# Performance work log

Hardware: AMD Instinct MI355X
Metric: run time of the kernel (lower is better)

The kernel has to match this reference:

```python
import jax, jax.numpy as jnp
import numpy as np

N = 50000
E = 640000
H = 128
C = 3

def _xavier(key, shape, gain=1.0):
    fan_in, fan_out = shape[0], shape[1]
    a = gain * np.sqrt(6.0 / (fan_in + fan_out))
    return jax.random.uniform(key, shape, jnp.float32, -a, a)

def setup_inputs() -> dict:
    key = jax.random.key(0)
    ks = jax.random.split(key, 12)
    h = jax.random.normal(ks[0], (N, H), jnp.float32)
    x = jax.random.normal(ks[1], (N, C), jnp.float32)
    edge_index = jax.random.randint(ks[2], (2, E), 0, N, jnp.int64 if jax.config.jax_enable_x64 else jnp.int32)
    # edge_mlp: Linear(2H+1 -> H), SiLU, Linear(H -> H), SiLU
    We1 = _xavier(ks[3], (2 * H + 1, H)); be1 = jnp.zeros((H,), jnp.float32)
    We2 = _xavier(ks[4], (H, H));          be2 = jnp.zeros((H,), jnp.float32)
    # coord_mlp: Linear(H -> H), SiLU, Linear(H -> 1, no bias, gain 0.01)
    Wc1 = _xavier(ks[5], (H, H)); bc1 = jnp.zeros((H,), jnp.float32)
    Wc2 = _xavier(ks[6], (H, 1), gain=0.01)
    # node_mlp: Linear(2H -> H), SiLU, Linear(H -> H)
    Wn1 = _xavier(ks[7], (2 * H, H)); bn1 = jnp.zeros((H,), jnp.float32)
    Wn2 = _xavier(ks[8], (H, H));     bn2 = jnp.zeros((H,), jnp.float32)
    return dict(h=h, x=x, edge_index=edge_index,
                We1=We1, be1=be1, We2=We2, be2=be2,
                Wc1=Wc1, bc1=bc1, Wc2=Wc2,
                Wn1=Wn1, bn1=bn1, Wn2=Wn2, bn2=bn2)

def reference(h, x, edge_index, We1, be1, We2, be2, Wc1, bc1, Wc2, Wn1, bn1, Wn2, bn2):
    src, dst = edge_index[0], edge_index[1]
    n = h.shape[0]
    rel_pos = x[src] - x[dst]                              # [E, C]
    dist_sq = jnp.sum(rel_pos * rel_pos, axis=-1, keepdims=True)  # [E, 1]
    edge_input = jnp.concatenate([h[src], h[dst], dist_sq], axis=-1)  # [E, 2H+1]
    m_ij = jax.nn.silu(edge_input @ We1 + be1)
    m_ij = jax.nn.silu(m_ij @ We2 + be2)                   # [E, H]
    coord_weight = jax.nn.silu(m_ij @ Wc1 + bc1) @ Wc2     # [E, 1]
    coord_agg = jax.ops.segment_sum(rel_pos * coord_weight, dst, num_segments=n)
    x_out = x + coord_agg
    msg_agg = jax.ops.segment_sum(m_ij, dst, num_segments=n)  # [N, H]
    node_input = jnp.concatenate([h, msg_agg], axis=-1)    # [N, 2H]
    h_upd = jax.nn.silu(node_input @ Wn1 + bn1) @ Wn2 + bn2
    h_out = h + h_upd
    return (h_out, x_out)
```

## Files before the change

### kernel.cpp

```cpp
#include <hip/hip_runtime.h>

#define H 128

typedef __bf16 bf8_t __attribute__((ext_vector_type(8)));
typedef __bf16 bf2_t __attribute__((ext_vector_type(2)));
typedef float  f4_t  __attribute__((ext_vector_type(4)));

#define MFMA16(a, b, c) __builtin_amdgcn_mfma_f32_16x16x32_bf16((a), (b), (c), 0, 0, 0)

__device__ __forceinline__ float silu_f(float v) {
    return v * (1.0f / (1.0f + __expf(-v)));
}

__device__ __forceinline__ void bar_lds() {
    asm volatile("s_waitcnt lgkmcnt(0)\ns_barrier" ::: "memory");
}

__device__ __forceinline__ float wload(const void* p, int idx, bool f32) {
    return f32 ? ((const float*)p)[idx] : (float)((const __bf16*)p)[idx];
}

__device__ __forceinline__ bf8_t hload8(const void* p, size_t off, bool f32) {
    bf8_t v;
    if (f32) {
        const float4* q = (const float4*)((const float*)p + off);
        const float4 a = q[0], b = q[1];
        v[0]=(__bf16)a.x; v[1]=(__bf16)a.y; v[2]=(__bf16)a.z; v[3]=(__bf16)a.w;
        v[4]=(__bf16)b.x; v[5]=(__bf16)b.y; v[6]=(__bf16)b.z; v[7]=(__bf16)b.w;
    } else {
        v = *(const bf8_t*)((const __bf16*)p + off);
    }
    return v;
}

__device__ __forceinline__ int eidx(const void* ei, int i, bool i64) {
    return i64 ? (int)((const long long*)ei)[i] : ((const int*)ei)[i];
}

__global__ void detect_kernel(const unsigned short* __restrict__ hraw,
                              const int* __restrict__ eiraw, int* __restrict__ flags)
{
    __shared__ int s_nf, s_oddnz;
    if (threadIdx.x == 0) { s_nf = 0; s_oddnz = 0; }
    __syncthreads();
    int nf = 0;
    for (int i = threadIdx.x; i < 16384; i += blockDim.x) {
        const unsigned short u = hraw[i];
        if (((u >> 7) & 0xFF) == 0xFF) nf++;
    }
    int onz = 0;
    for (int i = threadIdx.x; i < 512; i += blockDim.x) {
        if (eiraw[2*i + 1] != 0) onz++;
    }
    if (nf)  atomicAdd(&s_nf, nf);
    if (onz) atomicAdd(&s_oddnz, onz);
    __syncthreads();
    if (threadIdx.x == 0) {
        flags[0] = (s_nf > 0) ? 1 : 0;
        flags[1] = (s_oddnz == 0) ? 1 : 0;
    }
}

__global__ void histd_kernel(const void* __restrict__ ei, int* __restrict__ cnt,
                             const int* __restrict__ flags, int Ee)
{
    const int e = blockIdx.x*blockDim.x + threadIdx.x;
    if (e < Ee) atomicAdd(&cnt[eidx(ei, Ee + e, flags[1] != 0)], 1);
}

__global__ void scanA_kernel(const int* __restrict__ cnt, int* __restrict__ bsum, int Nn)
{
    __shared__ int s[512];
    const int gi = blockIdx.x*512 + threadIdx.x;
    s[threadIdx.x] = (gi < Nn) ? cnt[gi] : 0;
    __syncthreads();
    for (int off = 256; off > 0; off >>= 1) {
        if (threadIdx.x < off) s[threadIdx.x] += s[threadIdx.x + off];
        __syncthreads();
    }
    if (threadIdx.x == 0) bsum[blockIdx.x] = s[0];
}

__global__ void scanB_kernel(int* __restrict__ bsum, int* __restrict__ base, int nCh)
{
    if (threadIdx.x == 0) {
        int acc = 0;
        for (int b = 0; b < nCh; ++b) { base[b] = acc; acc += bsum[b]; }
    }
}
// ... 66 lines not shown
        #pragma unroll
        for (int kc = 0; kc < 4; ++kc) {
            bf8_t v;
            #pragma unroll
            for (int j = 0; j < 8; ++j)
                v[j] = (__bf16)wload(We1, (rb + kc*32 + quad*8 + j)*H + col, f32);
            bW[kc][t] = v;
        }
        bias[t] = (n < 128) ? 0.f : wload(be1, col, f32);
    }

    __shared__ __bf16 s_h[32*136];

    const int tiles = (Nn + 31) >> 5;
    for (int tile = blockIdx.x; tile < tiles; tile += gridDim.x) {
        const int nb = tile << 5;
        __syncthreads();
        {
            const int m = tid >> 4, c = tid & 15;
            int node = nb + m; if (node >= Nn) node = Nn - 1;
            *(bf8_t*)&s_h[m*136 + c*8] = hload8(h, (size_t)node*H + c*8, f32);
        }
        __syncthreads();

        f4_t acc[2][2];
        #pragma unroll
        for (int mm = 0; mm < 2; ++mm)
            #pragma unroll
            for (int t = 0; t < 2; ++t) acc[mm][t] = (f4_t){0.f,0.f,0.f,0.f};
        #pragma unroll
        for (int kc = 0; kc < 4; ++kc) {
            #pragma unroll
            for (int mm = 0; mm < 2; ++mm) {
                const bf8_t a = *(const bf8_t*)&s_h[(mm*16 + l15)*136 + quad*8 + kc*32];
                acc[mm][0] = MFMA16(a, bW[kc][0], acc[mm][0]);
                acc[mm][1] = MFMA16(a, bW[kc][1], acc[mm][1]);
            }
        }
        #pragma unroll
        for (int mm = 0; mm < 2; ++mm)
            #pragma unroll
            for (int i = 0; i < 4; ++i) {
                const int row = nb + mm*16 + quad*4 + i;
                if (row < Nn) {
                    #pragma unroll
                    for (int t = 0; t < 2; ++t)
                        PB[(size_t)row*256 + wv*32 + t*16 + l15] =
                            (__bf16)(acc[mm][t][i] + bias[t]);
                }
            }
    }
}

__global__ __launch_bounds__(512, 2)
void egnn_edge_pipe_kernel(const __bf16* __restrict__ PB,
                           const int* __restrict__ srcs, const int* __restrict__ dsts,
                           const float4* __restrict__ rel4,
                           const void* __restrict__ We1,
                           const void* __restrict__ We2, const void* __restrict__ be2,
                           const void* __restrict__ Wc1, const void* __restrict__ bc1,
                           const void* __restrict__ Wc2, const int* __restrict__ flags,
                           float* __restrict__ msg, float* __restrict__ coord,
                           int Ee)
{
    const bool f32 = flags[0] != 0;
    const int tid  = threadIdx.x;
    const int wv   = tid >> 6;
    const int lane = tid & 63;
    const int quad = lane >> 4;
    const int l15  = lane & 15;
    const int mg   = wv >> 2;
    const int ng   = wv & 3;

    bf8_t bW2[4][2], bWc[4][2];
    float be2v[2], bc1v[2], wc2v[2];
    #pragma unroll
    for (int t = 0; t < 2; ++t) {
        const int n = ng*32 + t*16 + l15;
        #pragma unroll
        for (int kc = 0; kc < 4; ++kc) {
            bf8_t v, u;
            #pragma unroll
            for (int j = 0; j < 8; ++j) {
                v[j] = (__bf16)wload(We2, (kc*32 + quad*8 + j)*H + n, f32);
                u[j] = (__bf16)wload(Wc1, (kc*32 + quad*8 + j)*H + n, f32);
            }
            bW2[kc][t] = v;
            bWc[kc][t] = u;
        }
        be2v[t] = wload(be2, n, f32);
        bc1v[t] = wload(bc1, n, f32);
        wc2v[t] = wload(Wc2, n, f32);
    }

    const int em = tid >> 3;
    const int ch = tid & 7;
    float w1dA[8], w1dB[8];
    #pragma unroll
    for (int j = 0; j < 8; ++j) {
        w1dA[j] = wload(We1, 256*H + ch*8 + j, f32);
        w1dB[j] = wload(We1, 256*H + (ch+8)*8 + j, f32);
    }

    __shared__ __bf16 s_m1[64*136];
    __shared__ __bf16 s_m2[64*136];
    __shared__ float  s_cw[4*64];
    __shared__ int    s_dst[2][64];
    __shared__ float4 s_rl[2][64];
    __shared__ float  s_pre[8][128];
    __shared__ float  s_suf[8][128];
    __shared__ int    s_wh[8];

    const int tiles = (Ee + 63) >> 6;
    const float* rw = (const float*)rel4;

    bf8_t rA0, rA1, rB0, rB1;
    float d2cur, d2nxt;
    int   s_n, d_n, d_c;
    float4 r4c, r4n;
    {
        int e0 = blockIdx.x*64 + em; if (e0 >= Ee) e0 = Ee - 1;
        const int sc = srcs[e0], dc = dsts[e0];
        d_c = dc;
        d2cur = rw[(size_t)e0*4 + 3];
        if (ch == 0) r4c = rel4[e0];
        rA0 = *(const bf8_t*)(PB + (size_t)sc*256 + ch*8);
        rA1 = *(const bf8_t*)(PB + (size_t)sc*256 + (ch+8)*8);
        rB0 = *(const bf8_t*)(PB + (size_t)dc*256 + 128 + ch*8);
        rB1 = *(const bf8_t*)(PB + (size_t)dc*256 + 128 + (ch+8)*8);
        const int t1 = blockIdx.x + gridDim.x;
        const int tt = (t1 < tiles) ? t1 : blockIdx.x;
        int e1 = tt*64 + em; if (e1 >= Ee) e1 = Ee - 1;
        s_n = srcs[e1]; d_n = dsts[e1]; d2nxt = rw[(size_t)e1*4 + 3];
        if (ch == 0) r4n = rel4[e1];
    }

    int li = 0;
    for (int t = blockIdx.x; t < tiles; t += gridDim.x, ++li) {
        const int sb = li & 1;
        {
            bf8_t o0, o1;
            #pragma unroll
            for (int j = 0; j < 8; ++j) {
                const float f0 = (float)rA0[j] + (float)rB0[j] + d2cur*w1dA[j];
                const float f1 = (float)rA1[j] + (float)rB1[j] + d2cur*w1dB[j];
                o0[j] = (__bf16)silu_f(f0);
                o1[j] = (__bf16)silu_f(f1);
            }
            *(bf8_t*)&s_m1[em*136 + ch*8]       = o0;
            *(bf8_t*)&s_m1[em*136 + (ch+8)*8]   = o1;
            if (ch == 0) { s_dst[sb][em] = d_c; s_rl[sb][em] = r4c; }
        }
        {
            const int sc = s_n, dc2 = d_n;
            rA0 = *(const bf8_t*)(PB + (size_t)sc*256 + ch*8);
            rA1 = *(const bf8_t*)(PB + (size_t)sc*256 + (ch+8)*8);
            rB0 = *(const bf8_t*)(PB + (size_t)dc2*256 + 128 + ch*8);
            rB1 = *(const bf8_t*)(PB + (size_t)dc2*256 + 128 + (ch+8)*8);
            d_c = d_n; d2cur = d2nxt;
            if (ch == 0) r4c = r4n;
            const int t2 = t + 2*gridDim.x;
            const int tt = (t2 < tiles) ? t2 : t;
            int e2 = tt*64 + em; if (e2 >= Ee) e2 = Ee - 1;
            s_n = srcs[e2]; d_n = dsts[e2]; d2nxt = rw[(size_t)e2*4 + 3];
            if (ch == 0) r4n = rel4[e2];
        }
        bar_lds();

        {
            f4_t a2[2][2];
            #pragma unroll
            for (int mm = 0; mm < 2; ++mm)
                #pragma unroll
                for (int h2 = 0; h2 < 2; ++h2) a2[mm][h2] = (f4_t){0.f,0.f,0.f,0.f};
            #pragma unroll
            for (int kc = 0; kc < 4; ++kc) {
                #pragma unroll
                for (int mm = 0; mm < 2; ++mm) {
                    const bf8_t a = *(const bf8_t*)&s_m1[(mg*32 + mm*16 + l15)*136 + quad*8 + kc*32];
                    a2[mm][0] = MFMA16(a, bW2[kc][0], a2[mm][0]);
                    a2[mm][1] = MFMA16(a, bW2[kc][1], a2[mm][1]);
                }
            }
            #pragma unroll
            for (int mm = 0; mm < 2; ++mm)
                #pragma unroll
                for (int i = 0; i < 4; ++i) {
                    const int m = mg*32 + mm*16 + quad*4 + i;
                    s_m2[m*136 + ng*32 + l15]      = (__bf16)silu_f(a2[mm][0][i] + be2v[0]);
                    s_m2[m*136 + ng*32 + 16 + l15] = (__bf16)silu_f(a2[mm][1][i] + be2v[1]);
                }
        }
        bar_lds();

        {
            f4_t a3[2][2];
            #pragma unroll
            for (int mm = 0; mm < 2; ++mm)
                #pragma unroll
                for (int h2 = 0; h2 < 2; ++h2) a3[mm][h2] = (f4_t){0.f,0.f,0.f,0.f};
            #pragma unroll
            for (int kc = 0; kc < 4; ++kc) {
                #pragma unroll
                for (int mm = 0; mm < 2; ++mm) {
                    const bf8_t a = *(const bf8_t*)&s_m2[(mg*32 + mm*16 + l15)*136 + quad*8 + kc*32];
                    a3[mm][0] = MFMA16(a, bWc[kc][0], a3[mm][0]);
                    a3[mm][1] = MFMA16(a, bWc[kc][1], a3[mm][1]);
                }
            }
            float p[2][4];
            #pragma unroll
            for (int mm = 0; mm < 2; ++mm)
                #pragma unroll
                for (int i = 0; i < 4; ++i) {
                    const float v0 = silu_f(a3[mm][0][i] + bc1v[0]);
                    const float v1 = silu_f(a3[mm][1][i] + bc1v[1]);
                    p[mm][i] = v0*wc2v[0] + v1*wc2v[1];
                }
            #pragma unroll
            for (int off = 1; off < 16; off <<= 1)
                #pragma unroll
                for (int mm = 0; mm < 2; ++mm)
                    #pragma unroll
                    for (int i = 0; i < 4; ++i) p[mm][i] += __shfl_xor(p[mm][i], off, 64);
            if (l15 == 0) {
                #pragma unroll
                for (int mm = 0; mm < 2; ++mm)
                    #pragma unroll
                    for (int i = 0; i < 4; ++i)
                        s_cw[ng*64 + (mg*32 + mm*16 + quad*4 + i)] = p[mm][i];
            }
        }

        {
            const int rbase = wv << 3;
            const int c0    = lane << 1;
            int   curd = __builtin_amdgcn_readfirstlane(s_dst[sb][rbase]);
            float ax = 0.f, ay = 0.f;
            float px = 0.f, py = 0.f;
            int   predone = 0;
            #pragma unroll
            for (int i = 0; i < 8; ++i) {
                const int d = __builtin_amdgcn_readfirstlane(s_dst[sb][rbase + i]);
                const bf2_t v = *(const bf2_t*)&s_m2[(rbase + i)*136 + c0];
                const float vx = (float)v[0], vy = (float)v[1];
                if (d != curd) {
                    if (!predone) { px = ax; py = ay; predone = 1; }
                    else {
                        float2 st; st.x = ax; st.y = ay;
                        *(float2*)&msg[(size_t)curd*H + c0] = st;
                    }
                    curd = d; ax = vx; ay = vy;
                } else { ax += vx; ay += vy; }
            }
            s_pre[wv][c0]   = px;  s_pre[wv][c0+1] = py;
            s_suf[wv][c0]   = ax;  s_suf[wv][c0+1] = ay;
            if (lane == 0) s_wh[wv] = !predone;
        }
        bar_lds();

        if (tid >= 128 && tid < 256) {
            const int c = tid - 128;
            int   curd2 = __builtin_amdgcn_readfirstlane(s_dst[sb][0]);
            float cur   = 0.f;
            int   first = 1;
            #pragma unroll
            for (int gg = 0; gg < 8; ++gg) {
                const int F  = __builtin_amdgcn_readfirstlane(s_dst[sb][gg*8]);
                const int L  = __builtin_amdgcn_readfirstlane(s_dst[sb][gg*8 + 7]);
                const int wh = __builtin_amdgcn_readfirstlane(s_wh[gg]);
                const float preg = s_pre[gg][c];
                const float sufg = s_suf[gg][c];
                if (F != curd2) {
                    if (first) atomicAdd(&msg[(size_t)curd2*H + c], cur);
                    else       msg[(size_t)curd2*H + c] = cur;
                    first = 0; curd2 = F; cur = 0.f;
                }
                if (wh) {
                    cur += sufg;
                } else {
                    cur += preg;
                    if (first) atomicAdd(&msg[(size_t)curd2*H + c], cur);
                    else       msg[(size_t)curd2*H + c] = cur;
                    first = 0; curd2 = L; cur = sufg;
                }
            }
            atomicAdd(&msg[(size_t)curd2*H + c], cur);
        }

        if (tid < 64) {
            const int e = tid;
            const float cwv = s_cw[e] + s_cw[64 + e] + s_cw[128 + e] + s_cw[192 + e];
            const float4 r = s_rl[sb][e];
            const int d = s_dst[sb][e];
            float vx = r.x*cwv, vy = r.y*cwv, vz = r.z*cwv;
            int   cn = 1;
            #pragma unroll
            for (int k = 1; k < 64; k <<= 1) {
                const int   dk = __shfl_up(d,  k, 64);
                const float xk = __shfl_up(vx, k, 64);
                const float yk = __shfl_up(vy, k, 64);
                const float zk = __shfl_up(vz, k, 64);
                const int   ck = __shfl_up(cn, k, 64);
                if (e >= k && dk == d) { vx += xk; vy += yk; vz += zk; cn += ck; }
            }
            const int dnx = __shfl_down(d, 1, 64);
            const bool runend = (e == 63) || (dnx != d);
            if (runend) {
                const int rs = e - cn + 1;
                if (rs == 0 || e == 63) {
                    atomicAdd(&coord[(size_t)d*3 + 0], vx);
                    atomicAdd(&coord[(size_t)d*3 + 1], vy);
                    atomicAdd(&coord[(size_t)d*3 + 2], vz);
                } else {
                    coord[(size_t)d*3 + 0] = vx;
                    coord[(size_t)d*3 + 1] = vy;
                    coord[(size_t)d*3 + 2] = vz;
                }
            }
        }
    }
}

__global__ __launch_bounds__(512, 2)
void egnn_node_kernel(const void* __restrict__ h, const float* __restrict__ msg,
                      const void* __restrict__ Wn1, const void* __restrict__ bn1,
                      const void* __restrict__ Wn2, const void* __restrict__ bn2,
                      const int* __restrict__ flags, void* __restrict__ h_out,
                      const void* __restrict__ x, const float* __restrict__ coord,
                      size_t obase, int do_x, int Nn)
{
    const bool f32 = flags[0] != 0;
    const int tid  = threadIdx.x;
    const int wv   = tid >> 6;
    const int lane = tid & 63;
    const int quad = lane >> 4;
    const int l15  = lane & 15;
    const int mg   = wv >> 2;
    const int ng   = wv & 3;

    bf8_t bW1[8][2];
    bf8_t bW2[4][2];
    float b1v[2], b2v[2];
    #pragma unroll
    for (int t = 0; t < 2; ++t) {
        const int n = ng*32 + t*16 + l15;
        #pragma unroll
        for (int kc = 0; kc < 8; ++kc) {
            bf8_t v;
            #pragma unroll
            for (int j = 0; j < 8; ++j) v[j] = (__bf16)wload(Wn1, (kc*32 + quad*8 + j)*H + n, f32);
            bW1[kc][t] = v;
        }
        #pragma unroll
        for (int kc = 0; kc < 4; ++kc) {
            bf8_t v;
            #pragma unroll
            for (int j = 0; j < 8; ++j) v[j] = (__bf16)wload(Wn2, (kc*32 + quad*8 + j)*H + n, f32);
            bW2[kc][t] = v;
        }
        b1v[t] = wload(bn1, n, f32);
        b2v[t] = wload(bn2, n, f32);
    }

    __shared__ __bf16 s_in[32*264];
    __shared__ __bf16 s_t1[32*136];

    const int tiles = (Nn + 31) >> 5;
    for (int tile = blockIdx.x; tile < tiles; tile += gridDim.x) {
        const int nb = tile << 5;
        __syncthreads();
        #pragma unroll
        for (int r = 0; r < 2; ++r) {
// ... 238 lines not shown
                #pragma unroll
                for (int i = 0; i < 4; ++i)
                    s_cw[(mg*16 + quad*4 + i)*4 + ng] = p[i];
            }
        }
        __syncthreads();

        if (tid < 96) {
            const int m = tid / 3, c = tid - m*3;
            const float cw = s_cw[m*4 + 0] + s_cw[m*4 + 1] + s_cw[m*4 + 2] + s_cw[m*4 + 3];
            atomicAdd(&coord_agg[(size_t)s_dstv[m]*3 + c], s_rel[m*3 + c]*cw);
        }
    }
}

__global__ void egnn_x_kernel(const void* __restrict__ x, const float* __restrict__ coord_agg,
                              const int* __restrict__ flags, void* __restrict__ out,
                              size_t obase, int total)
{
    const bool f32 = flags[0] != 0;
    const int i = blockIdx.x*blockDim.x + threadIdx.x;
    if (i >= total) return;
    const float xv = f32 ? ((const float*)x)[i] : (float)((const __bf16*)x)[i];
    const float o = xv + coord_agg[i];
    if (f32) ((float*)out)[obase + i] = o;
    else     ((__bf16*)out)[obase + i] = (__bf16)o;
}

static inline size_t align256(size_t v) { return (v + 255) & ~(size_t)255; }

extern "C" void kernel_launch(void* const* d_in, const int* in_sizes, int n_in,
                              void* d_out, int out_size, void* d_ws, size_t ws_size,
                              hipStream_t stream)
{
    const void* h   = d_in[0];
    const void* x   = d_in[1];
    const void* ei0 = d_in[2];
    const void* We1 = d_in[3];
    const void* be1 = d_in[4];
    const void* We2 = d_in[5];
    const void* be2 = d_in[6];
    const void* Wc1 = d_in[7];
    const void* bc1 = d_in[8];
    const void* Wc2 = d_in[9];
    const void* Wn1 = d_in[10];
    const void* bn1 = d_in[11];
    const void* Wn2 = d_in[12];
    const void* bn2 = d_in[13];

    const int Nn = in_sizes[0] / H;
    const int Ee = in_sizes[2] / 2;

    char* ws = (char*)d_ws;
    size_t o = 0;
    size_t o_cnt   = o; o = align256(o + (size_t)Nn*4);
    size_t o_msg   = o; o = align256(o + (size_t)Nn*H*4);
    size_t o_coord = o; o = align256(o + (size_t)Nn*3*4);
    const size_t zero_end = o;
    size_t o_srcs  = o; o = align256(o + (size_t)Ee*4);
    size_t o_dsts  = o; o = align256(o + (size_t)Ee*4);
    size_t o_rel   = o; o = align256(o + (size_t)Ee*16);
    size_t o_pb    = o; o = align256(o + (size_t)Nn*256*2);
    size_t o_off   = o; o = align256(o + (size_t)(Nn+1)*4);
    size_t o_cur   = o; o = align256(o + (size_t)Nn*4);
    size_t o_bsum  = o; o = align256(o + 512*4);
    size_t o_base  = o; o = align256(o + 512*4);
    size_t o_flags = o; o = align256(o + 64);
    const size_t need_csr = o;

    const int nCh = (Nn + 1 + 511) / 512;

    if (ws_size >= need_csr) {
        int*    cnt     = (int*)   (ws + o_cnt);
        float*  msg     = (float*) (ws + o_msg);
        float*  coord   = (float*) (ws + o_coord);
        int*    srcs    = (int*)   (ws + o_srcs);
        int*    dsts    = (int*)   (ws + o_dsts);
        float4* rel4    = (float4*)(ws + o_rel);
        __bf16* PB      = (__bf16*)(ws + o_pb);
        int*    off     = (int*)   (ws + o_off);
        int*    cursor  = (int*)   (ws + o_cur);
        int*    bsum    = (int*)   (ws + o_bsum);
        int*    base    = (int*)   (ws + o_base);
        int*    flags   = (int*)   (ws + o_flags);

        detect_kernel<<<1, 256, 0, stream>>>((const unsigned short*)h, (const int*)ei0, flags);
        hipMemsetAsync(ws + o_cnt, 0, zero_end - o_cnt, stream);
        histd_kernel<<<(Ee + 511)/512, 512, 0, stream>>>(ei0, cnt, flags, Ee);
        scanA_kernel<<<nCh, 512, 0, stream>>>(cnt, bsum, Nn);
        scanB_kernel<<<1, 64, 0, stream>>>(bsum, base, nCh);
        scanC_kernel<<<nCh, 512, 0, stream>>>(cnt, base, off, cursor, Nn);
        scatgeo_kernel<<<(Ee + 511)/512, 512, 0, stream>>>(ei0, cursor, srcs, dsts,
                                                           rel4, x, flags, Ee);
        proj_kernel<<<512, 512, 0, stream>>>(h, We1, be1, flags, PB, Nn);

        egnn_edge_pipe_kernel<<<512, 512, 0, stream>>>(PB, srcs, dsts, rel4,
                                                       We1, We2, be2, Wc1, bc1, Wc2,
                                                       flags, msg, coord, Ee);

        egnn_node_kernel<<<1024, 512, 0, stream>>>(h, msg, Wn1, bn1, Wn2, bn2,
                                                   flags, d_out, x, coord,
                                                   (size_t)Nn*H, 1, Nn);
    } else {
        float* msg_agg   = (float*)ws;
        float* coord_agg = (float*)(ws + (size_t)Nn*H*4);
        int*   ei        = (int*)  (ws + (size_t)Nn*H*4 + (size_t)Nn*3*4);
        int*   flags     = (int*)  (ws + (size_t)Nn*H*4 + (size_t)Nn*3*4 + (size_t)2*Ee*4);

        detect_kernel<<<1, 256, 0, stream>>>((const unsigned short*)h, (const int*)ei0, flags);
        cvt_ei_kernel<<<(2*Ee + 255)/256, 256, 0, stream>>>(ei0, ei, 2*Ee, flags);
        hipMemsetAsync(msg_agg,   0, (size_t)Nn*H*4, stream);
        hipMemsetAsync(coord_agg, 0, (size_t)Nn*3*4, stream);
        egnn_edge_kernel<<<1024, 512, 0, stream>>>(h, x, ei, We1, be1, We2, be2,
                                                   Wc1, bc1, Wc2, flags,
                                                   msg_agg, coord_agg, Nn, Ee);
        egnn_node_kernel<<<512, 512, 0, stream>>>(h, msg_agg, Wn1, bn1, Wn2, bn2,
                                                  flags, d_out, x, coord_agg,
                                                  (size_t)Nn*H, 0, Nn);
        egnn_x_kernel<<<(Nn*3 + 255)/256, 256, 0, stream>>>(x, coord_agg, flags, d_out,
                                                            (size_t)Nn*H, Nn*3);
    }
}
```

Measured before the change: 652.9 us.

## Materialize per-edge messages and gather-reduce them in CSR node kernel

Adds a new edge kernel that writes each edge's bf16 message vector and partial coordinate weights to a workspace buffer instead of doing segmented reductions in-kernel. A new node kernel then sums each node's messages along CSR offsets and fuses the coordinate aggregation and node MLP, so the msg/coord memsets and float accumulation buffers are no longer needed. In exchange it writes and rereads roughly 256 bytes per edge of extra global traffic and needs a larger workspace. It falls back to the old path if the workspace is too small.

```diff
diff --git a/kernel.cpp b/kernel.cpp
--- a/kernel.cpp
+++ b/kernel.cpp
@@ -208,6 +208,345 @@
 }
 
 __global__ __launch_bounds__(512, 2)
+void egnn_edge_pipe2_kernel(const __bf16* __restrict__ PB,
+                            const int* __restrict__ srcs, const int* __restrict__ dsts,
+                            const float4* __restrict__ rel4,
+                            const void* __restrict__ We1,
+                            const void* __restrict__ We2, const void* __restrict__ be2,
+                            const void* __restrict__ Wc1, const void* __restrict__ bc1,
+                            const void* __restrict__ Wc2, const int* __restrict__ flags,
+                            unsigned int* __restrict__ m_buf,
+                            float* __restrict__ cwp,
+                            int Ee)
+{
+    const bool f32 = flags[0] != 0;
+    const int tid  = threadIdx.x;
+    const int wv   = tid >> 6;
+    const int lane = tid & 63;
+    const int quad = lane >> 4;
+    const int l15  = lane & 15;
+    const int mg   = wv >> 2;
+    const int ng   = wv & 3;
+
+    bf8_t bW2[4][2], bWc[4][2];
+    float be2v[2], bc1v[2], wc2v[2];
+    #pragma unroll
+    for (int t = 0; t < 2; ++t) {
+        const int n = ng*32 + t*16 + l15;
+        #pragma unroll
+        for (int kc = 0; kc < 4; ++kc) {
+            bf8_t v, u;
+            #pragma unroll
+            for (int j = 0; j < 8; ++j) {
+                v[j] = (__bf16)wload(We2, (kc*32 + quad*8 + j)*H + n, f32);
+                u[j] = (__bf16)wload(Wc1, (kc*32 + quad*8 + j)*H + n, f32);
+            }
+            bW2[kc][t] = v;
+            bWc[kc][t] = u;
+        }
+        be2v[t] = wload(be2, n, f32);
+        bc1v[t] = wload(bc1, n, f32);
+        wc2v[t] = wload(Wc2, n, f32);
+    }
+
+    const int em = tid >> 3;
+    const int ch = tid & 7;
+    float w1dA[8], w1dB[8];
+    #pragma unroll
+    for (int j = 0; j < 8; ++j) {
+        w1dA[j] = wload(We1, 256*H + ch*8 + j, f32);
+        w1dB[j] = wload(We1, 256*H + (ch+8)*8 + j, f32);
+    }
+
+    __shared__ __bf16 s_m1[64*136];
+    __shared__ __bf16 s_m2[64*136];
+
+    const int tiles = (Ee + 63) >> 6;
+    const float* rw = (const float*)rel4;
+
+    bf8_t rA0, rA1, rB0, rB1;
+    float d2cur, d2nxt;
+    int   s_n, d_n;
+    {
+        int e0 = blockIdx.x*64 + em; if (e0 >= Ee) e0 = Ee - 1;
+        const int sc = srcs[e0], dc = dsts[e0];
+        d2cur = rw[(size_t)e0*4 + 3];
+        rA0 = *(const bf8_t*)(PB + (size_t)sc*256 + ch*8);
+        rA1 = *(const bf8_t*)(PB + (size_t)sc*256 + (ch+8)*8);
+        rB0 = *(const bf8_t*)(PB + (size_t)dc*256 + 128 + ch*8);
+        rB1 = *(const bf8_t*)(PB + (size_t)dc*256 + 128 + (ch+8)*8);
+        const int t1 = blockIdx.x + gridDim.x;
+        const int tt = (t1 < tiles) ? t1 : blockIdx.x;
+        int e1 = tt*64 + em; if (e1 >= Ee) e1 = Ee - 1;
+        s_n = srcs[e1]; d_n = dsts[e1]; d2nxt = rw[(size_t)e1*4 + 3];
+    }
+
+    for (int t = blockIdx.x; t < tiles; t += gridDim.x) {
+        {
+            bf8_t o0, o1;
+            #pragma unroll
+            for (int j = 0; j < 8; ++j) {
+                const float f0 = (float)rA0[j] + (float)rB0[j] + d2cur*w1dA[j];
+                const float f1 = (float)rA1[j] + (float)rB1[j] + d2cur*w1dB[j];
+                o0[j] = (__bf16)silu_f(f0);
+                o1[j] = (__bf16)silu_f(f1);
+            }
+            *(bf8_t*)&s_m1[em*136 + ch*8]       = o0;
+            *(bf8_t*)&s_m1[em*136 + (ch+8)*8]   = o1;
+        }
+        {
+            const int sc = s_n, dc2 = d_n;
+            rA0 = *(const bf8_t*)(PB + (size_t)sc*256 + ch*8);
+            rA1 = *(const bf8_t*)(PB + (size_t)sc*256 + (ch+8)*8);
+            rB0 = *(const bf8_t*)(PB + (size_t)dc2*256 + 128 + ch*8);
+            rB1 = *(const bf8_t*)(PB + (size_t)dc2*256 + 128 + (ch+8)*8);
+            d2cur = d2nxt;
+            const int t2 = t + 2*gridDim.x;
+            const int tt = (t2 < tiles) ? t2 : t;
+            int e2 = tt*64 + em; if (e2 >= Ee) e2 = Ee - 1;
+            s_n = srcs[e2]; d_n = dsts[e2]; d2nxt = rw[(size_t)e2*4 + 3];
+        }
+        bar_lds();
+
+        {
+            f4_t a2[2][2];
+            #pragma unroll
+            for (int mm = 0; mm < 2; ++mm)
+                #pragma unroll
+                for (int h2 = 0; h2 < 2; ++h2) a2[mm][h2] = (f4_t){0.f,0.f,0.f,0.f};
+            __builtin_amdgcn_s_setprio(1);
+            #pragma unroll
+            for (int kc = 0; kc < 4; ++kc) {
+                #pragma unroll
+                for (int mm = 0; mm < 2; ++mm) {
+                    const bf8_t a = *(const bf8_t*)&s_m1[(mg*32 + mm*16 + l15)*136 + quad*8 + kc*32];
+                    a2[mm][0] = MFMA16(a, bW2[kc][0], a2[mm][0]);
+                    a2[mm][1] = MFMA16(a, bW2[kc][1], a2[mm][1]);
+                }
+            }
+            __builtin_amdgcn_s_setprio(0);
+            #pragma unroll
+            for (int mm = 0; mm < 2; ++mm)
+                #pragma unroll
+                for (int i = 0; i < 4; ++i) {
+                    const int m = mg*32 + mm*16 + quad*4 + i;
+                    const float v0 = silu_f(a2[mm][0][i] + be2v[0]);
+                    const float v1 = silu_f(a2[mm][1][i] + be2v[1]);
+                    const __bf16 b0 = (__bf16)v0, b1 = (__bf16)v1;
+                    s_m2[m*136 + ng*32 + l15]      = b0;
+                    s_m2[m*136 + ng*32 + 16 + l15] = b1;
+                    const unsigned int w =
+                        ((unsigned int)__builtin_bit_cast(unsigned short, b1) << 16) |
+                        (unsigned int)__builtin_bit_cast(unsigned short, b0);
+                    m_buf[(size_t)(t*64 + m)*64 + ng*16 + l15] = w;
+                }
+        }
+        bar_lds();
+
+        {
+            f4_t a3[2][2];
+            #pragma unroll
+            for (int mm = 0; mm < 2; ++mm)
+                #pragma unroll
+                for (int h2 = 0; h2 < 2; ++h2) a3[mm][h2] = (f4_t){0.f,0.f,0.f,0.f};
+            __builtin_amdgcn_s_setprio(1);
+            #pragma unroll
+            for (int kc = 0; kc < 4; ++kc) {
+                #pragma unroll
+                for (int mm = 0; mm < 2; ++mm) {
+                    const bf8_t a = *(const bf8_t*)&s_m2[(mg*32 + mm*16 + l15)*136 + quad*8 + kc*32];
+                    a3[mm][0] = MFMA16(a, bWc[kc][0], a3[mm][0]);
+                    a3[mm][1] = MFMA16(a, bWc[kc][1], a3[mm][1]);
+                }
+            }
+            __builtin_amdgcn_s_setprio(0);
+            float p[2][4];
+            #pragma unroll
+            for (int mm = 0; mm < 2; ++mm)
+                #pragma unroll
+                for (int i = 0; i < 4; ++i) {
+                    const float v0 = silu_f(a3[mm][0][i] + bc1v[0]);
+                    const float v1 = silu_f(a3[mm][1][i] + bc1v[1]);
+                    p[mm][i] = v0*wc2v[0] + v1*wc2v[1];
+                }
+            #pragma unroll
+            for (int off = 1; off < 16; off <<= 1)
+                #pragma unroll
+                for (int mm = 0; mm < 2; ++mm)
+                    #pragma unroll
+                    for (int i = 0; i < 4; ++i) p[mm][i] += __shfl_xor(p[mm][i], off, 64);
+            if (l15 == 0) {
+                #pragma unroll
+                for (int mm = 0; mm < 2; ++mm)
+                    #pragma unroll
+                    for (int i = 0; i < 4; ++i)
+                        cwp[(size_t)(t*64 + mg*32 + mm*16 + quad*4 + i)*4 + ng] = p[mm][i];
+            }
+        }
+    }
+}
+
+__global__ __launch_bounds__(512, 2)
+void egnn_node_csr_kernel(const void* __restrict__ h,
+                          const unsigned int* __restrict__ m_buf,
+                          const int* __restrict__ offv,
+                          const void* __restrict__ Wn1, const void* __restrict__ bn1,
+                          const void* __restrict__ Wn2, const void* __restrict__ bn2,
+                          const int* __restrict__ flags, void* __restrict__ h_out,
+                          const void* __restrict__ x, const float4* __restrict__ rel4,
+                          const float* __restrict__ cwp,
+                          size_t obase, int Nn)
+{
+    const bool f32 = flags[0] != 0;
+    const int tid  = threadIdx.x;
+    const int wv   = tid >> 6;
+    const int lane = tid & 63;
+    const int quad = lane >> 4;
+    const int l15  = lane & 15;
+    const int mg   = wv >> 2;
+    const int ng   = wv & 3;
+
+    bf8_t bW1[8][2];
+    bf8_t bW2[4][2];
+    float b1v[2], b2v[2];
+    #pragma unroll
+    for (int t = 0; t < 2; ++t) {
+        const int n = ng*32 + t*16 + l15;
+        #pragma unroll
+        for (int kc = 0; kc < 8; ++kc) {
+            bf8_t v;
+            #pragma unroll
+            for (int j = 0; j < 8; ++j) {
+                const int P = kc*32 + quad*8 + j;
+                int krow;
+                if (P < 128) krow = P;
+                else {
+                    const int e2 = P - 128;
+                    const int cp = e2 >> 1, s = e2 & 1;
+                    krow = 128 + ((cp >> 4)*32 + (cp & 15) + 16*s);
+                }
+                v[j] = (__bf16)wload(Wn1, krow*H + n, f32);
+            }
+            bW1[kc][t] = v;
+        }
+        #pragma unroll
+        for (int kc = 0; kc < 4; ++kc) {
+            bf8_t v;
+            #pragma unroll
+            for (int j = 0; j < 8; ++j) v[j] = (__bf16)wload(Wn2, (kc*32 + quad*8 + j)*H + n, f32);
+            bW2[kc][t] = v;
+        }
+        b1v[t] = wload(bn1, n, f32);
+        b2v[t] = wload(bn2, n, f32);
+    }
+
+    __shared__ __bf16 s_in[32*264];
+    __shared__ __bf16 s_t1[32*136];
+
+    const int tiles = (Nn + 31) >> 5;
+    for (int tile = blockIdx.x; tile < tiles; tile += gridDim.x) {
+        const int nb = tile << 5;
+        __syncthreads();
+        {
+            const int m = tid >> 4, c = tid & 15;
+            int node = nb + m; if (node >= Nn) node = Nn - 1;
+            *(bf8_t*)&s_in[m*264 + c*8] = hload8(h, (size_t)node*H + c*8, f32);
+        }
+        {
+            const int m = tid >> 4, cp8 = tid & 15;
+            int node = nb + m; if (node >= Nn) node = Nn - 1;
+            const int p0 = offv[node], p1 = offv[node+1];
+            float acc[8];
+            #pragma unroll
+            for (int k = 0; k < 8; ++k) acc[k] = 0.f;
+            const uint4* mp = (const uint4*)m_buf;
+            for (int p = p0; p < p1; ++p) {
+                const uint4 w = mp[(size_t)p*16 + cp8];
+                acc[0] += __uint_as_float(w.x << 16);
+                acc[1] += __uint_as_float(w.x & 0xffff0000u);
+                acc[2] += __uint_as_float(w.y << 16);
+                acc[3] += __uint_as_float(w.y & 0xffff0000u);
+                acc[4] += __uint_as_float(w.z << 16);
+                acc[5] += __uint_as_float(w.z & 0xffff0000u);
+                acc[6] += __uint_as_float(w.w << 16);
+                acc[7] += __uint_as_float(w.w & 0xffff0000u);
+            }
+            __bf16* d = &s_in[m*264 + 128 + cp8*8];
+            #pragma unroll
+            for (int k = 0; k < 8; ++k) d[k] = (__bf16)acc[k];
+        }
+        if (tid < 96) {
+            const int m = tid / 3, c = tid - m*3;
+            const int node = nb + m;
+            if (node < Nn) {
+                const int p0 = offv[node], p1 = offv[node+1];
+                float acc = 0.f;
+                for (int p = p0; p < p1; ++p) {
+                    const float4 c4 = *(const float4*)&cwp[(size_t)p*4];
+                    const float cw = (c4.x + c4.y) + (c4.z + c4.w);
+                    const float4 r = rel4[p];
+                    const float rc = (c == 0) ? r.x : (c == 1) ? r.y : r.z;
+                    acc += rc * cw;
+                }
+                const float xv = wload(x, node*3 + c, f32);
+                const float o = xv + acc;
+                if (f32) ((float*)h_out)[obase + (size_t)node*3 + c] = o;
+                else     ((__bf16*)h_out)[obase + (size_t)node*3 + c] = (__bf16)o;
+            }
+        }
+        __syncthreads();
+
+        {
+            f4_t a0 = {0.f,0.f,0.f,0.f}, a1 = {0.f,0.f,0.f,0.f};
+            const int abase = (mg*16 + l15)*264 + quad*8;
+            #pragma unroll
+            for (int kc = 0; kc < 8; ++kc) {
+                const bf8_t a = *(const bf8_t*)&s_in[abase + kc*32];
+                a0 = MFMA16(a, bW1[kc][0], a0);
+                a1 = MFMA16(a, bW1[kc][1], a1);
+            }
+            #pragma unroll
+            for (int i = 0; i < 4; ++i) {
+                const int m = mg*16 + quad*4 + i;
+                s_t1[m*136 + ng*32 + l15]      = (__bf16)silu_f(a0[i] + b1v[0]);
+                s_t1[m*136 + ng*32 + 16 + l15] = (__bf16)silu_f(a1[i] + b1v[1]);
+            }
+        }
+        __syncthreads();
+
+        {
+            f4_t a0 = {0.f,0.f,0.f,0.f}, a1 = {0.f,0.f,0.f,0.f};
+            const int abase = (mg*16 + l15)*136 + quad*8;
+            #pragma unroll
+            for (int kc = 0; kc < 4; ++kc) {
+                const bf8_t a = *(const bf8_t*)&s_t1[abase + kc*32];
+                a0 = MFMA16(a, bW2[kc][0], a0);
+                a1 = MFMA16(a, bW2[kc][1], a1);
+            }
+            #pragma unroll
+            for (int i = 0; i < 4; ++i) {
+                const int node = nb + mg*16 + quad*4 + i;
+                if (node < Nn) {
+                    const int n0 = ng*32 + l15, n1 = n0 + 16;
+                    const size_t i0 = (size_t)node*H + n0, i1 = (size_t)node*H + n1;
+                    const float h0 = f32 ? ((const float*)h)[i0] : (float)((const __bf16*)h)[i0];
+                    const float h1 = f32 ? ((const float*)h)[i1] : (float)((const __bf16*)h)[i1];
+                    const float o0 = a0[i] + b2v[0] + h0;
+                    const float o1 = a1[i] + b2v[1] + h1;
+                    if (f32) {
+                        ((float*)h_out)[i0] = o0;
+                        ((float*)h_out)[i1] = o1;
+                    } else {
+                        ((__bf16*)h_out)[i0] = (__bf16)o0;
+                        ((__bf16*)h_out)[i1] = (__bf16)o1;
+                    }
+                }
+            }
+        }
+    }
+}
+
+__global__ __launch_bounds__(512, 2)
 void egnn_edge_pipe_kernel(const __bf16* __restrict__ PB,
                            const int* __restrict__ srcs, const int* __restrict__ dsts,
                            const float4* __restrict__ rel4,
@@ -256,6 +595,11 @@
         w1dA[j] = wload(We1, 256*H + ch*8 + j, f32);
         w1dB[j] = wload(We1, 256*H + (ch+8)*8 + j, f32);
     }
+
+    const int rcol = tid >> 2;
+    const int rg   = tid & 3;
+    const int qb   = lane & ~3;
+    (void)rcol; (void)rg; (void)qb;
 
     __shared__ __bf16 s_m1[64*136];
     __shared__ __bf16 s_m2[64*136];
@@ -818,6 +1162,60 @@
     const int Ee = in_sizes[2] / 2;
 
     char* ws = (char*)d_ws;
+    const int nCh = (Nn + 1 + 511) / 512;
+
+    {
+        size_t o = 0;
+        size_t o_cnt   = o; o = align256(o + (size_t)Nn*4);
+        size_t o_srcs  = o; o = align256(o + (size_t)Ee*4);
+        size_t o_dsts  = o; o = align256(o + (size_t)Ee*4);
+        size_t o_rel   = o; o = align256(o + (size_t)Ee*16);
+        size_t o_pb    = o; o = align256(o + (size_t)Nn*256*2);
+        size_t o_off   = o; o = align256(o + (size_t)(Nn+1)*4);
+        size_t o_cur   = o; o = align256(o + (size_t)Nn*4);
+        size_t o_bsum  = o; o = align256(o + 512*4);
+        size_t o_base  = o; o = align256(o + 512*4);
+        size_t o_flags = o; o = align256(o + 64);
+        size_t o_mbuf  = o; o = align256(o + (size_t)Ee*256);
+        size_t o_cwp   = o; o = align256(o + (size_t)Ee*16);
+        const size_t need_new = o;
+
+        if (ws_size >= need_new) {
+            int*    cnt     = (int*)   (ws + o_cnt);
+            int*    srcs    = (int*)   (ws + o_srcs);
+            int*    dsts    = (int*)   (ws + o_dsts);
+            float4* rel4    = (float4*)(ws + o_rel);
+            __bf16* PB      = (__bf16*)(ws + o_pb);
+            int*    off     = (int*)   (ws + o_off);
+            int*    cursor  = (int*)   (ws + o_cur);
+            int*    bsum    = (int*)   (ws + o_bsum);
+            int*    base    = (int*)   (ws + o_base);
+            int*    flags   = (int*)   (ws + o_flags);
+            unsigned int* m_buf = (unsigned int*)(ws + o_mbuf);
+            float*  cwp     = (float*) (ws + o_cwp);
+
+            detect_kernel<<<1, 256, 0, stream>>>((const unsigned short*)h, (const int*)ei0, flags);
+            hipMemsetAsync(cnt, 0, (size_t)Nn*4, stream);
+            histd_kernel<<<(Ee + 511)/512, 512, 0, stream>>>(ei0, cnt, flags, Ee);
+            scanA_kernel<<<nCh, 512, 0, stream>>>(cnt, bsum, Nn);
+            scanB_kernel<<<1, 64, 0, stream>>>(bsum, base, nCh);
+            scanC_kernel<<<nCh, 512, 0, stream>>>(cnt, base, off, cursor, Nn);
+            scatgeo_kernel<<<(Ee + 511)/512, 512, 0, stream>>>(ei0, cursor, srcs, dsts,
+                                                               rel4, x, flags, Ee);
+            proj_kernel<<<512, 512, 0, stream>>>(h, We1, be1, flags, PB, Nn);
+
+            egnn_edge_pipe2_kernel<<<512, 512, 0, stream>>>(PB, srcs, dsts, rel4,
+                                                            We1, We2, be2, Wc1, bc1, Wc2,
+                                                            flags, m_buf, cwp, Ee);
+
+            egnn_node_csr_kernel<<<1024, 512, 0, stream>>>(h, m_buf, off,
+                                                           Wn1, bn1, Wn2, bn2,
+                                                           flags, d_out, x, rel4, cwp,
+                                                           (size_t)Nn*H, Nn);
+            return;
+        }
+    }
+
     size_t o = 0;
     size_t o_cnt   = o; o = align256(o + (size_t)Nn*4);
     size_t o_msg   = o; o = align256(o + (size_t)Nn*H*4);
@@ -834,8 +1232,6 @@
     size_t o_flags = o; o = align256(o + 64);
     const size_t need_csr = o;
 
-    const int nCh = (Nn + 1 + 511) / 512;
-
     if (ws_size >= need_csr) {
         int*    cnt     = (int*)   (ws + o_cnt);
         float*  msg     = (float*) (ws + o_msg);
```

New measurement: 750.0 us. +14.9%, slower.

## Restructure edge kernel to per-wave 16-edge tiles without block barriers

Applied to the files above, without the earlier changes.

Replaces the block-cooperative 64-edge tile pipeline with a design where each wave independently processes 16 edges. Weights for the two 128x128 MFMAs are staged once in LDS, using a transposed MFMA formulation so edge data stays in registers. Per-wave segmented reductions replace the block-wide prefix/suffix combine, which removes all per-tile block barriers. In exchange, every MFMA now reads its weight fragments from LDS, and the shorter tiles may issue more atomics at run boundaries.

```diff
diff --git a/kernel.cpp b/kernel.cpp
--- a/kernel.cpp
+++ b/kernel.cpp
@@ -3,17 +3,12 @@
 #define H 128
 
 typedef __bf16 bf8_t __attribute__((ext_vector_type(8)));
-typedef __bf16 bf2_t __attribute__((ext_vector_type(2)));
 typedef float  f4_t  __attribute__((ext_vector_type(4)));
 
 #define MFMA16(a, b, c) __builtin_amdgcn_mfma_f32_16x16x32_bf16((a), (b), (c), 0, 0, 0)
 
 __device__ __forceinline__ float silu_f(float v) {
     return v * (1.0f / (1.0f + __expf(-v)));
-}
-
-__device__ __forceinline__ void bar_lds() {
-    asm volatile("s_waitcnt lgkmcnt(0)\ns_barrier" ::: "memory");
 }
 
 __device__ __forceinline__ float wload(const void* p, int idx, bool f32) {
@@ -35,6 +30,12 @@
 
 __device__ __forceinline__ int eidx(const void* ei, int i, bool i64) {
     return i64 ? (int)((const long long*)ei)[i] : ((const int*)ei)[i];
+}
+
+__device__ __forceinline__ unsigned int pkbf(float a, float b) {
+    const __bf16 x = (__bf16)a, y = (__bf16)b;
+    return ((unsigned int)__builtin_bit_cast(unsigned short, y) << 16) |
+           (unsigned int)__builtin_bit_cast(unsigned short, x);
 }
 
 __global__ void detect_kernel(const unsigned short* __restrict__ hraw,
@@ -207,8 +208,8 @@
     }
 }
 
-__global__ __launch_bounds__(512, 2)
-void egnn_edge_pipe_kernel(const __bf16* __restrict__ PB,
+__global__ __launch_bounds__(1024)
+void egnn_edge_wave_kernel(const __bf16* __restrict__ PB,
                            const int* __restrict__ srcs, const int* __restrict__ dsts,
                            const float4* __restrict__ rel4,
                            const void* __restrict__ We1,
@@ -224,246 +225,197 @@
     const int lane = tid & 63;
     const int quad = lane >> 4;
     const int l15  = lane & 15;
-    const int mg   = wv >> 2;
-    const int ng   = wv & 3;
-
-    bf8_t bW2[4][2], bWc[4][2];
-    float be2v[2], bc1v[2], wc2v[2];
-    #pragma unroll
-    for (int t = 0; t < 2; ++t) {
-        const int n = ng*32 + t*16 + l15;
+
+    __shared__ __align__(16) __bf16 s_w2[2048*8];
+    __shared__ __align__(16) __bf16 s_wc[2048*8];
+    __shared__ __align__(16) float  s_bias[4][128];
+    __shared__ __align__(16) __bf16 s_m2w[16][16*152];
+
+    for (int f = tid; f < 2048; f += 1024) {
+        const int g = f >> 8, kc = (f >> 6) & 3, ln = f & 63;
+        const int qd = ln >> 4, l = ln & 15;
+        bf8_t v, u;
+        #pragma unroll
+        for (int j = 0; j < 8; ++j) {
+            const int k = kc*32 + qd*8 + j;
+            v[j] = (__bf16)wload(We2, k*H + g*16 + l, f32);
+            u[j] = (__bf16)wload(Wc1, k*H + g*16 + l, f32);
+        }
+        *(bf8_t*)&s_w2[f*8] = v;
+        *(bf8_t*)&s_wc[f*8] = u;
+    }
+    if (tid < 512) {
+        const int a = tid >> 7, c = tid & 127;
+        float v;
+        if      (a == 0) v = wload(We1, 256*H + c, f32);
+        else if (a == 1) v = wload(be2, c, f32);
+        else if (a == 2) v = wload(bc1, c, f32);
+        else             v = wload(Wc2, c, f32);
+        s_bias[a][c] = v;
+    }
+    __syncthreads();
+
+    const int tiles  = (Ee + 15) >> 4;
+    const int stride = gridDim.x * 16;
+    const float* rw  = (const float*)rel4;
+    int mt = blockIdx.x*16 + wv;
+    if (mt >= tiles) return;
+
+    int e0 = mt*16 + l15; if (e0 >= Ee) e0 = Ee - 1;
+    float d2c = rw[(size_t)e0*4 + 3];
+    int dval;
+    bf8_t rS[4], rD[4];
+    {
+        const int sc = srcs[e0], dc = dsts[e0];
+        dval = (mt*16 + l15 < Ee) ? dc : -1;
         #pragma unroll
         for (int kc = 0; kc < 4; ++kc) {
-            bf8_t v, u;
-            #pragma unroll
-            for (int j = 0; j < 8; ++j) {
-                v[j] = (__bf16)wload(We2, (kc*32 + quad*8 + j)*H + n, f32);
-                u[j] = (__bf16)wload(Wc1, (kc*32 + quad*8 + j)*H + n, f32);
-            }
-            bW2[kc][t] = v;
-            bWc[kc][t] = u;
-        }
-        be2v[t] = wload(be2, n, f32);
-        bc1v[t] = wload(bc1, n, f32);
-        wc2v[t] = wload(Wc2, n, f32);
-    }
-
-    const int em = tid >> 3;
-    const int ch = tid & 7;
-    float w1dA[8], w1dB[8];
-    #pragma unroll
-    for (int j = 0; j < 8; ++j) {
-        w1dA[j] = wload(We1, 256*H + ch*8 + j, f32);
-        w1dB[j] = wload(We1, 256*H + (ch+8)*8 + j, f32);
-    }
-
-    __shared__ __bf16 s_m1[64*136];
-    __shared__ __bf16 s_m2[64*136];
-    __shared__ float  s_cw[4*64];
-    __shared__ int    s_dst[2][64];
-    __shared__ float4 s_rl[2][64];
-    __shared__ float  s_pre[8][128];
-    __shared__ float  s_suf[8][128];
-    __shared__ int    s_wh[8];
-
-    const int tiles = (Ee + 63) >> 6;
-    const float* rw = (const float*)rel4;
-
-    bf8_t rA0, rA1, rB0, rB1;
-    float d2cur, d2nxt;
-    int   s_n, d_n, d_c;
-    float4 r4c, r4n;
-    {
-        int e0 = blockIdx.x*64 + em; if (e0 >= Ee) e0 = Ee - 1;
-        const int sc = srcs[e0], dc = dsts[e0];
-        d_c = dc;
-        d2cur = rw[(size_t)e0*4 + 3];
-        if (ch == 0) r4c = rel4[e0];
-        rA0 = *(const bf8_t*)(PB + (size_t)sc*256 + ch*8);
-        rA1 = *(const bf8_t*)(PB + (size_t)sc*256 + (ch+8)*8);
-        rB0 = *(const bf8_t*)(PB + (size_t)dc*256 + 128 + ch*8);
-        rB1 = *(const bf8_t*)(PB + (size_t)dc*256 + 128 + (ch+8)*8);
-        const int t1 = blockIdx.x + gridDim.x;
-        const int tt = (t1 < tiles) ? t1 : blockIdx.x;
-        int e1 = tt*64 + em; if (e1 >= Ee) e1 = Ee - 1;
-        s_n = srcs[e1]; d_n = dsts[e1]; d2nxt = rw[(size_t)e1*4 + 3];
-        if (ch == 0) r4n = rel4[e1];
-    }
-
-    int li = 0;
-    for (int t = blockIdx.x; t < tiles; t += gridDim.x, ++li) {
-        const int sb = li & 1;
+            rS[kc] = *(const bf8_t*)(PB + (size_t)sc*256 + kc*32 + quad*8);
+            rD[kc] = *(const bf8_t*)(PB + (size_t)dc*256 + 128 + kc*32 + quad*8);
+        }
+    }
+
+    for (; mt < tiles; mt += stride) {
+        const int mtn = mt + stride;
+        int e1 = mtn*16 + l15; if (e1 >= Ee) e1 = Ee - 1;
+        const int sn = srcs[e1], dn = dsts[e1];
+        const float d2n = rw[(size_t)e1*4 + 3];
+        const int dvn = (mtn*16 + l15 < Ee) ? dn : -1;
+
+        bf8_t m1f[4];
+        #pragma unroll
+        for (int kc = 0; kc < 4; ++kc) {
+            const f4_t w0 = *(const f4_t*)&s_bias[0][kc*32 + quad*8];
+            const f4_t w1 = *(const f4_t*)&s_bias[0][kc*32 + quad*8 + 4];
+            bf8_t m;
+            #pragma unroll
+            for (int j = 0; j < 4; ++j) {
+                const float f = (float)rS[kc][j] + (float)rD[kc][j] + d2c*w0[j];
+                m[j] = (__bf16)silu_f(f);
+            }
+            #pragma unroll
+            for (int j = 4; j < 8; ++j) {
+                const float f = (float)rS[kc][j] + (float)rD[kc][j] + d2c*w1[j-4];
+                m[j] = (__bf16)silu_f(f);
+            }
+            m1f[kc] = m;
+        }
+
         {
-            bf8_t o0, o1;
-            #pragma unroll
-            for (int j = 0; j < 8; ++j) {
-                const float f0 = (float)rA0[j] + (float)rB0[j] + d2cur*w1dA[j];
-                const float f1 = (float)rA1[j] + (float)rB1[j] + d2cur*w1dB[j];
-                o0[j] = (__bf16)silu_f(f0);
-                o1[j] = (__bf16)silu_f(f1);
-            }
-            *(bf8_t*)&s_m1[em*136 + ch*8]       = o0;
-            *(bf8_t*)&s_m1[em*136 + (ch+8)*8]   = o1;
-            if (ch == 0) { s_dst[sb][em] = d_c; s_rl[sb][em] = r4c; }
-        }
-        {
-            const int sc = s_n, dc2 = d_n;
-            rA0 = *(const bf8_t*)(PB + (size_t)sc*256 + ch*8);
-            rA1 = *(const bf8_t*)(PB + (size_t)sc*256 + (ch+8)*8);
-            rB0 = *(const bf8_t*)(PB + (size_t)dc2*256 + 128 + ch*8);
-            rB1 = *(const bf8_t*)(PB + (size_t)dc2*256 + 128 + (ch+8)*8);
-            d_c = d_n; d2cur = d2nxt;
-            if (ch == 0) r4c = r4n;
-            const int t2 = t + 2*gridDim.x;
-            const int tt = (t2 < tiles) ? t2 : t;
-            int e2 = tt*64 + em; if (e2 >= Ee) e2 = Ee - 1;
-            s_n = srcs[e2]; d_n = dsts[e2]; d2nxt = rw[(size_t)e2*4 + 3];
-            if (ch == 0) r4n = rel4[e2];
-        }
-        bar_lds();
-
-        {
-            f4_t a2[2][2];
-            #pragma unroll
-            for (int mm = 0; mm < 2; ++mm)
-                #pragma unroll
-                for (int h2 = 0; h2 < 2; ++h2) a2[mm][h2] = (f4_t){0.f,0.f,0.f,0.f};
+            f4_t acc[8];
+            #pragma unroll
+            for (int g = 0; g < 8; ++g)
+                acc[g] = *(const f4_t*)&s_bias[1][g*16 + quad*4];
             #pragma unroll
             for (int kc = 0; kc < 4; ++kc) {
                 #pragma unroll
-                for (int mm = 0; mm < 2; ++mm) {
-                    const bf8_t a = *(const bf8_t*)&s_m1[(mg*32 + mm*16 + l15)*136 + quad*8 + kc*32];
-                    a2[mm][0] = MFMA16(a, bW2[kc][0], a2[mm][0]);
-                    a2[mm][1] = MFMA16(a, bW2[kc][1], a2[mm][1]);
+                for (int g = 0; g < 8; ++g) {
+                    const bf8_t wf = *(const bf8_t*)&s_w2[((g*4 + kc)*64 + lane)*8];
+                    acc[g] = MFMA16(wf, m1f[kc], acc[g]);
                 }
             }
             #pragma unroll
-            for (int mm = 0; mm < 2; ++mm)
+            for (int g = 0; g < 8; ++g) {
+                const float v0 = silu_f(acc[g][0]);
+                const float v1 = silu_f(acc[g][1]);
+                const float v2 = silu_f(acc[g][2]);
+                const float v3 = silu_f(acc[g][3]);
+                uint2 w; w.x = pkbf(v0, v1); w.y = pkbf(v2, v3);
+                *(uint2*)&s_m2w[wv][l15*152 + g*16 + quad*4] = w;
+            }
+        }
+
+        #pragma unroll
+        for (int kc = 0; kc < 4; ++kc) {
+            rS[kc] = *(const bf8_t*)(PB + (size_t)sn*256 + kc*32 + quad*8);
+            rD[kc] = *(const bf8_t*)(PB + (size_t)dn*256 + 128 + kc*32 + quad*8);
+        }
+
+        float cw;
+        {
+            f4_t a3[8];
+            #pragma unroll
+            for (int g = 0; g < 8; ++g)
+                a3[g] = *(const f4_t*)&s_bias[2][g*16 + quad*4];
+            #pragma unroll
+            for (int kc = 0; kc < 4; ++kc) {
+                const bf8_t bm = *(const bf8_t*)&s_m2w[wv][l15*152 + kc*32 + quad*8];
                 #pragma unroll
-                for (int i = 0; i < 4; ++i) {
-                    const int m = mg*32 + mm*16 + quad*4 + i;
-                    s_m2[m*136 + ng*32 + l15]      = (__bf16)silu_f(a2[mm][0][i] + be2v[0]);
-                    s_m2[m*136 + ng*32 + 16 + l15] = (__bf16)silu_f(a2[mm][1][i] + be2v[1]);
+                for (int g = 0; g < 8; ++g) {
+                    const bf8_t wf = *(const bf8_t*)&s_wc[((g*4 + kc)*64 + lane)*8];
+                    a3[g] = MFMA16(wf, bm, a3[g]);
                 }
-        }
-        bar_lds();
+            }
+            float p = 0.f;
+            #pragma unroll
+            for (int g = 0; g < 8; ++g) {
+                const f4_t wc = *(const f4_t*)&s_bias[3][g*16 + quad*4];
+                #pragma unroll
+                for (int i = 0; i < 4; ++i)
+                    p += silu_f(a3[g][i]) * wc[i];
+            }
+            p += __shfl_xor(p, 16, 64);
+            p += __shfl_xor(p, 32, 64);
+            cw = p;
+        }
 
         {
-            f4_t a3[2][2];
-            #pragma unroll
-            for (int mm = 0; mm < 2; ++mm)
-                #pragma unroll
-                for (int h2 = 0; h2 < 2; ++h2) a3[mm][h2] = (f4_t){0.f,0.f,0.f,0.f};
-            #pragma unroll
-            for (int kc = 0; kc < 4; ++kc) {
-                #pragma unroll
-                for (int mm = 0; mm < 2; ++mm) {
-                    const bf8_t a = *(const bf8_t*)&s_m2[(mg*32 + mm*16 + l15)*136 + quad*8 + kc*32];
-                    a3[mm][0] = MFMA16(a, bWc[kc][0], a3[mm][0]);
-                    a3[mm][1] = MFMA16(a, bWc[kc][1], a3[mm][1]);
-                }
-            }
-            float p[2][4];
-            #pragma unroll
-            for (int mm = 0; mm < 2; ++mm)
-                #pragma unroll
-                for (int i = 0; i < 4; ++i) {
-                    const float v0 = silu_f(a3[mm][0][i] + bc1v[0]);
-                    const float v1 = silu_f(a3[mm][1][i] + bc1v[1]);
-                    p[mm][i] = v0*wc2v[0] + v1*wc2v[1];
-                }
-            #pragma unroll
-            for (int off = 1; off < 16; off <<= 1)
-                #pragma unroll
-                for (int mm = 0; mm < 2; ++mm)
-                    #pragma unroll
-                    for (int i = 0; i < 4; ++i) p[mm][i] += __shfl_xor(p[mm][i], off, 64);
-            if (l15 == 0) {
-                #pragma unroll
-                for (int mm = 0; mm < 2; ++mm)
-                    #pragma unroll
-                    for (int i = 0; i < 4; ++i)
-                        s_cw[ng*64 + (mg*32 + mm*16 + quad*4 + i)] = p[mm][i];
-            }
-        }
-
-        {
-            const int rbase = wv << 3;
-            const int c0    = lane << 1;
-            int   curd = __builtin_amdgcn_readfirstlane(s_dst[sb][rbase]);
-            float ax = 0.f, ay = 0.f;
-            float px = 0.f, py = 0.f;
-            int   predone = 0;
-            #pragma unroll
-            for (int i = 0; i < 8; ++i) {
-                const int d = __builtin_amdgcn_readfirstlane(s_dst[sb][rbase + i]);
-                const bf2_t v = *(const bf2_t*)&s_m2[(rbase + i)*136 + c0];
-                const float vx = (float)v[0], vy = (float)v[1];
-                if (d != curd) {
-                    if (!predone) { px = ax; py = ay; predone = 1; }
-                    else {
-                        float2 st; st.x = ax; st.y = ay;
-                        *(float2*)&msg[(size_t)curd*H + c0] = st;
+            const int c0 = lane << 1;
+            const unsigned int* mw = (const unsigned int*)&s_m2w[wv][0];
+            int curd, first = 1;
+            float ax, ay;
+            {
+                curd = __builtin_amdgcn_readfirstlane(__shfl(dval, 0, 64));
+                const unsigned int w = mw[lane];
+                ax = __uint_as_float(w << 16);
+                ay = __uint_as_float(w & 0xffff0000u);
+            }
+            #pragma unroll
+            for (int i = 1; i < 16; ++i) {
+                const int di = __builtin_amdgcn_readfirstlane(__shfl(dval, i, 64));
+                const unsigned int w = mw[i*76 + lane];
+                const float vx = __uint_as_float(w << 16);
+                const float vy = __uint_as_float(w & 0xffff0000u);
+                if (di != curd) {
+                    if (curd >= 0) {
+                        if (first) {
+                            atomicAdd(&msg[(size_t)curd*H + c0],     ax);
+                            atomicAdd(&msg[(size_t)curd*H + c0 + 1], ay);
+                        } else {
+                            float2 st; st.x = ax; st.y = ay;
+                            *(float2*)&msg[(size_t)curd*H + c0] = st;
+                        }
                     }
-                    curd = d; ax = vx; ay = vy;
+                    first = 0;
+                    curd = di; ax = vx; ay = vy;
                 } else { ax += vx; ay += vy; }
             }
-            s_pre[wv][c0]   = px;  s_pre[wv][c0+1] = py;
-            s_suf[wv][c0]   = ax;  s_suf[wv][c0+1] = ay;
-            if (lane == 0) s_wh[wv] = !predone;
-        }
-        bar_lds();
-
-        if (tid >= 128 && tid < 256) {
-            const int c = tid - 128;
-            int   curd2 = __builtin_amdgcn_readfirstlane(s_dst[sb][0]);
-            float cur   = 0.f;
-            int   first = 1;
-            #pragma unroll
-            for (int gg = 0; gg < 8; ++gg) {
-                const int F  = __builtin_amdgcn_readfirstlane(s_dst[sb][gg*8]);
-                const int L  = __builtin_amdgcn_readfirstlane(s_dst[sb][gg*8 + 7]);
-                const int wh = __builtin_amdgcn_readfirstlane(s_wh[gg]);
-                const float preg = s_pre[gg][c];
-                const float sufg = s_suf[gg][c];
-                if (F != curd2) {
-                    if (first) atomicAdd(&msg[(size_t)curd2*H + c], cur);
-                    else       msg[(size_t)curd2*H + c] = cur;
-                    first = 0; curd2 = F; cur = 0.f;
-                }
-                if (wh) {
-                    cur += sufg;
-                } else {
-                    cur += preg;
-                    if (first) atomicAdd(&msg[(size_t)curd2*H + c], cur);
-                    else       msg[(size_t)curd2*H + c] = cur;
-                    first = 0; curd2 = L; cur = sufg;
-                }
-            }
-            atomicAdd(&msg[(size_t)curd2*H + c], cur);
-        }
-
-        if (tid < 64) {
-            const int e = tid;
-            const float cwv = s_cw[e] + s_cw[64 + e] + s_cw[128 + e] + s_cw[192 + e];
-            const float4 r = s_rl[sb][e];
-            const int d = s_dst[sb][e];
-            float vx = r.x*cwv, vy = r.y*cwv, vz = r.z*cwv;
-            int   cn = 1;
-            #pragma unroll
-            for (int k = 1; k < 64; k <<= 1) {
+            if (curd >= 0) {
+                atomicAdd(&msg[(size_t)curd*H + c0],     ax);
+                atomicAdd(&msg[(size_t)curd*H + c0 + 1], ay);
+            }
+        }
+
+        if (lane < 16) {
+            int e = mt*16 + lane; if (e >= Ee) e = Ee - 1;
+            const int d = dval;
+            const float4 r = rel4[e];
+            float vx = r.x*cw, vy = r.y*cw, vz = r.z*cw;
+            int cn = 1;
+            #pragma unroll
+            for (int k = 1; k < 16; k <<= 1) {
                 const int   dk = __shfl_up(d,  k, 64);
                 const float xk = __shfl_up(vx, k, 64);
                 const float yk = __shfl_up(vy, k, 64);
                 const float zk = __shfl_up(vz, k, 64);
                 const int   ck = __shfl_up(cn, k, 64);
-                if (e >= k && dk == d) { vx += xk; vy += yk; vz += zk; cn += ck; }
+                if (lane >= k && dk == d) { vx += xk; vy += yk; vz += zk; cn += ck; }
             }
             const int dnx = __shfl_down(d, 1, 64);
-            const bool runend = (e == 63) || (dnx != d);
-            if (runend) {
-                const int rs = e - cn + 1;
-                if (rs == 0 || e == 63) {
+            const bool runend = (lane == 15) || (dnx != d);
+            if (runend && d >= 0) {
+                const int rs = lane - cn + 1;
+                if (rs == 0 || lane == 15) {
                     atomicAdd(&coord[(size_t)d*3 + 0], vx);
                     atomicAdd(&coord[(size_t)d*3 + 1], vy);
                     atomicAdd(&coord[(size_t)d*3 + 2], vz);
@@ -474,6 +426,8 @@
                 }
             }
         }
+
+        d2c = d2n; dval = dvn;
     }
 }
 
@@ -860,9 +814,9 @@
                                                            rel4, x, flags, Ee);
         proj_kernel<<<512, 512, 0, stream>>>(h, We1, be1, flags, PB, Nn);
 
-        egnn_edge_pipe_kernel<<<512, 512, 0, stream>>>(PB, srcs, dsts, rel4,
-                                                       We1, We2, be2, Wc1, bc1, Wc2,
-                                                       flags, msg, coord, Ee);
+        egnn_edge_wave_kernel<<<256, 1024, 0, stream>>>(PB, srcs, dsts, rel4,
+                                                        We1, We2, be2, Wc1, bc1, Wc2,
+                                                        flags, msg, coord, Ee);
 
         egnn_node_kernel<<<1024, 512, 0, stream>>>(h, msg, Wn1, bn1, Wn2, bn2,
                                                    flags, d_out, x, coord,
```

Result: slower. 1.352 ms (+107.0%).
